# Performance work log

Measured on AMD Instinct MI355X. Metric: run time of the kernel, lower is better.

Reference implementation:

```python
import jax, jax.numpy as jnp
import numpy as np

N = 100000          # nodes
E = 1600000         # edges (avg degree 16)
F_IN = 35           # len(cfg.objects)
C = 21              # channels (out_channels)
DIMS = [F_IN, 16 * C, 8 * C, 4 * C, 2 * C]  # conv1..conv4 in-dims -> next
MAX_LOGSTD = 10.0


def setup_inputs() -> dict:
    key = jax.random.key(0)
    ks = jax.random.split(key, 16)
    inp = {
        "x": jax.random.normal(ks[0], (N, F_IN), dtype=jnp.float32),
        "edge_index": jax.random.randint(ks[1], (2, E), 0, N, dtype=jnp.int32),
        "eps": jax.random.normal(ks[2], (N, C), dtype=jnp.float32),
    }
    # GCNConv weights (glorot-ish scaling) and biases for conv1..conv4
    for i in range(4):
        din, dout = DIMS[i], DIMS[i + 1]
        inp[f"W{i+1}"] = jax.random.normal(ks[3 + i], (din, dout), dtype=jnp.float32) / np.sqrt(din)
        inp[f"b{i+1}"] = jnp.zeros((dout,), dtype=jnp.float32)
    # conv_mu / conv_logstd: 2*C -> C
    inp["W_mu"] = jax.random.normal(ks[8], (2 * C, C), dtype=jnp.float32) / np.sqrt(2 * C)
    inp["b_mu"] = jnp.zeros((C,), dtype=jnp.float32)
    inp["W_logstd"] = jax.random.normal(ks[9], (2 * C, C), dtype=jnp.float32) / np.sqrt(2 * C)
    inp["b_logstd"] = jnp.zeros((C,), dtype=jnp.float32)
    return inp


def _gcn_conv(x, src, dst, edge_norm, self_norm, W, b):
    # PyG GCNConv: linear transform first, then normalized scatter-add
    # (messages flow src -> dst, plus the self-loop term deg^-1/2 * deg^-1/2).
    h = x @ W                                            # [N, dout]
    msg = h[src] * edge_norm[:, None]                    # [E, dout] gather
    agg = jax.ops.segment_sum(msg, dst, num_segments=N)  # scatter-add
    agg = agg + h * self_norm[:, None]                   # self-loop contribution
    return agg + b


def reference(x, edge_index, eps, W1, b1, W2, b2, W3, b3, W4, b4,
              W_mu, b_mu, W_logstd, b_logstd):
    src, dst = edge_index[0], edge_index[1]
    # Symmetric normalization with self-loops: deg[i] = in_deg[i] + 1
    deg = jax.ops.segment_sum(jnp.ones((E,), x.dtype), dst, num_segments=N) + 1.0
    dinv = jax.lax.rsqrt(deg)                 # deg > 0 always (self loop)
    edge_norm = dinv[src] * dinv[dst]         # [E]
    self_norm = dinv * dinv                   # [N]

    h = jax.nn.relu(_gcn_conv(x, src, dst, edge_norm, self_norm, W1, b1))
    h = jax.nn.relu(_gcn_conv(h, src, dst, edge_norm, self_norm, W2, b2))
    h = jax.nn.relu(_gcn_conv(h, src, dst, edge_norm, self_norm, W3, b3))
    h = jax.nn.relu(_gcn_conv(h, src, dst, edge_norm, self_norm, W4, b4))

    mu = _gcn_conv(h, src, dst, edge_norm, self_norm, W_mu, b_mu)
    logstd = jnp.minimum(
        _gcn_conv(h, src, dst, edge_norm, self_norm, W_logstd, b_logstd),
        MAX_LOGSTD,
    )
    # VGAE reparameterize (training mode)
    z = mu + eps * jnp.exp(logstd)
    # Predictor
    p_z = jax.nn.log_softmax(z, axis=1)
    return p_z
```

## Files before the change

kernel.cpp:

```cpp
#include <hip/hip_runtime.h>

#define NN 100000
#define NE 1600000
#define MP 100096
#define NB 782
#define BSL 3072
#define CHUNK 8192

typedef short  short8 __attribute__((ext_vector_type(8)));
typedef float  f32x4  __attribute__((ext_vector_type(4)));
typedef float  f32x2  __attribute__((ext_vector_type(2)));

#if defined(__has_builtin)
# if __has_builtin(__builtin_amdgcn_cvt_pk_f32_fp8) && __has_builtin(__builtin_amdgcn_cvt_pk_fp8_f32)
#  define HW_FP8 1
# endif
#endif

__device__ __forceinline__ unsigned short f2bf(float f){
  unsigned int u = __float_as_uint(f);
  u += 0x7fffu + ((u >> 16) & 1u);
  return (unsigned short)(u >> 16);
}
__device__ __forceinline__ float bfl(unsigned int v){ return __uint_as_float((v & 0xffffu) << 16); }
__device__ __forceinline__ float bfh(unsigned int v){ return __uint_as_float(v & 0xffff0000u); }
__device__ __forceinline__ float bf1(unsigned short v){ return __uint_as_float(((unsigned int)v) << 16); }


__device__ __forceinline__ void dec4(unsigned int v, float f[4]){
#ifdef HW_FP8
  f32x2 lo = __builtin_amdgcn_cvt_pk_f32_fp8((int)v, false);
  f32x2 hi = __builtin_amdgcn_cvt_pk_f32_fp8((int)v, true);
  f[0] = lo[0]; f[1] = lo[1]; f[2] = hi[0]; f[3] = hi[1];
#else
  #pragma unroll
  for (int k = 0; k < 4; ++k){
    unsigned b = (v >> (8 * k)) & 0xffu;
    int em = b & 0x7f;
    float m = (em < 8) ? (float)em * 0.001953125f
                       : __uint_as_float((unsigned)((((em >> 3) + 120) << 23) | ((em & 7) << 20)));
    f[k] = (b & 0x80) ? -m : m;
  }
#endif
}

#ifndef HW_FP8
__device__ __forceinline__ unsigned int enc1m(float v){
  unsigned u = __float_as_uint(v);
  unsigned s = (u >> 24) & 0x80u;
  float av = fabsf(v);
  if (!(av >= 0.0009765625f)) return s;
  if (av >= 448.0f) return s | 0x7eu;
  if (av < 0.015625f){
    int q = (int)rintf(av * 512.0f);
    return s | (unsigned)q;
  }
  unsigned au = u & 0x7fffffffu;
  au += 0x7ffffu + ((au >> 20) & 1u);
  int ex = (int)(au >> 23) - 127;
  unsigned man = (au >> 20) & 7u;
  if (ex > 8) return s | 0x7eu;
  return s | (unsigned)((ex + 7) << 3) | man;
}
#endif

__device__ __forceinline__ unsigned int enc1(float v){
#ifdef HW_FP8
  return (unsigned int)__builtin_amdgcn_cvt_pk_fp8_f32(v, 0.0f, 0, false) & 0xffu;
#else
  return enc1m(v);
#endif
}

__device__ __forceinline__ unsigned int enc4(float a, float b, float c, float d){
#ifdef HW_FP8
  int lo = __builtin_amdgcn_cvt_pk_fp8_f32(a, b, 0, false);
  return (unsigned int)__builtin_amdgcn_cvt_pk_fp8_f32(c, d, lo, true);
#else
  return enc1m(a) | (enc1m(b) << 8) | (enc1m(c) << 16) | (enc1m(d) << 24);
#endif
}


__global__ __launch_bounds__(256) void k_bin1(const int* __restrict__ src, const int* __restrict__ dst,
                                              int* __restrict__ bcur, int2* __restrict__ tmp){
  __shared__ int cnt[NB];
  __shared__ int base[NB];
  __shared__ int pos[NB];
  int t = threadIdx.x;
  int e0 = blockIdx.x * CHUNK;
  int e1 = min(e0 + CHUNK, NE);
  for (int i = t; i < NB; i += 256){ cnt[i] = 0; pos[i] = 0; }
  __syncthreads();
  for (int e = e0 + t; e < e1; e += 256)
    atomicAdd(&cnt[dst[e] >> 7], 1);
  __syncthreads();
  for (int i = t; i < NB; i += 256){
    int c = cnt[i];
    base[i] = (c > 0) ? atomicAdd(&bcur[i], c) : 0;
  }
  __syncthreads();
  for (int e = e0 + t; e < e1; e += 256){
    int s = src[e], d = dst[e];
    int b = d >> 7;
    int p = b * BSL + base[b] + atomicAdd(&pos[b], 1);
    tmp[p] = make_int2(s, d);
  }
}

__global__ __launch_bounds__(256) void k_bscan(const int* __restrict__ bcur, int* __restrict__ bbase,
                                               int* __restrict__ rp){
  __shared__ int sh[256];
  int t = threadIdx.x;
  int b0 = t * 4;
  int v0 = (b0     < NB) ? bcur[b0]     : 0;
  int v1 = (b0 + 1 < NB) ? bcur[b0 + 1] : 0;
  int v2 = (b0 + 2 < NB) ? bcur[b0 + 2] : 0;
  int v3 = (b0 + 3 < NB) ? bcur[b0 + 3] : 0;
  int s = v0 + v1 + v2 + v3;
  sh[t] = s; __syncthreads();
  for (int off = 1; off < 256; off <<= 1){
    int val = sh[t];
    int add = (t >= off) ? sh[t - off] : 0;
    __syncthreads();
    sh[t] = val + add;
    __syncthreads();
  }
  int excl = sh[t] - s;
  if (b0     < NB) bbase[b0]     = excl;
  if (b0 + 1 < NB) bbase[b0 + 1] = excl + v0;
  if (b0 + 2 < NB) bbase[b0 + 2] = excl + v0 + v1;
  if (b0 + 3 < NB) bbase[b0 + 3] = excl + v0 + v1 + v2;
  if (t == 255){ bbase[NB] = sh[255]; rp[NN] = NE; }
}

__global__ __launch_bounds__(256) void k_bin2(const int2* __restrict__ tmp, const int* __restrict__ bbase,
                                              int* __restrict__ rp, float* __restrict__ dinv,
                                              int* __restrict__ cw){
  __shared__ int hist[128];
  __shared__ int cur[128];
  int b = blockIdx.x;
  int n0 = b << 7;
  int nn = min(128, NN - n0);
  int t = threadIdx.x;
  int B0 = bbase[b];
  int C  = bbase[b + 1] - B0;
  int E0 = b * BSL;
  if (t < 128) hist[t] = 0;
  __syncthreads();
  for (int e = t; e < C; e += 256)
    atomicAdd(&hist[tmp[E0 + e].y - n0], 1);
  __syncthreads();
  int val = (t < 128) ? hist[t] : 0;
  for (int off = 1; off < 128; off <<= 1){
    int add = (t < 128 && t >= off) ? hist[t - off] : 0;
    __syncthreads();
    if (t < 128) hist[t] += add;
    __syncthreads();
  }
  if (t < 128){
    int excl = hist[t] - val;
    int rpv = B0 + excl;
    cur[t] = rpv;
    if (t < nn){
      rp[n0 + t] = rpv;
      dinv[n0 + t] = rsqrtf((float)val + 1.0f);
    }
  }
  __syncthreads();
  for (int e = t; e < C; e += 256){
    int2 p = tmp[E0 + e];
    int slot = atomicAdd(&cur[p.y - n0], 1);
    cw[slot] = p.x;
  }
}


__device__ __forceinline__ void pack1(const float* __restrict__ W, unsigned short* __restrict__ dst,
                                      int din, int dout, int Np, int idx){
  int j = idx & 7;
  int l = (idx >> 3) & 63;
  int f = idx >> 9;
  int ntiles = Np >> 4;
  int nt = f % ntiles;
  int ks = f / ntiles;
  int k = ks * 32 + (l >> 4) * 8 + j;
  int n = nt * 16 + (l & 15);
  float v = (k < din && n < dout) ? W[k * dout + n] : 0.0f;
  dst[idx] = f2bf(v);
}

__global__ __launch_bounds__(256) void k_gxpack(const float* __restrict__ x, const float* __restrict__ dinv,
                                                unsigned int* __restrict__ gx,
                                                const float* __restrict__ W1, unsigned short* __restrict__ d1,
                                                const float* __restrict__ W2, unsigned short* __restrict__ d2,
                                                const float* __restrict__ W3, unsigned short* __restrict__ d3,
                                                const float* __restrict__ W4, unsigned short* __restrict__ d4){
  if (blockIdx.x < 6250){
    int idx = blockIdx.x * 256 + threadIdx.x;
    if (idx >= NN * 16) return;
    int row = idx >> 4;
    int cu  = idx & 15;
    float di = dinv[row];
    float v[4];
    #pragma unroll
    for (int k = 0; k < 4; ++k){
      int c = 4 * cu + k;
      v[k] = (c < 35) ? x[row * 35 + c] * di : 0.0f;
    }
    gx[idx] = enc4(v[0], v[1], v[2], v[3]);
  } else {
    int idx = (blockIdx.x - 6250) * 256 + threadIdx.x;
    if      (idx < 22528)  pack1(W1, d1, 35, 336, 352, idx);
    else if (idx < 90112)  pack1(W2, d2, 336, 168, 192, idx - 22528);
    else if (idx < 108544) pack1(W3, d3, 168, 84, 96, idx - 90112);
    else if (idx < 114688) pack1(W4, d4, 84, 42, 64, idx - 108544);
  }
}


template<int SPB, int OUTC, int DOUT, int MODE, int OUTF8>
__global__ __launch_bounds__(256) void k_aggf8(const unsigned char* __restrict__ Pin,
                                               void* __restrict__ Hout,
                                               const int* __restrict__ rp, const int* __restrict__ cw,
                                               const float* __restrict__ dinv, const float* __restrict__ bias){
  constexpr int L  = 16;
  constexpr int U  = SPB / 4;
  constexpr int CH = U / L;
  constexpr int UN = (CH == 1) ? 8 : 4;
  int g = blockIdx.x * 16 + (threadIdx.x >> 4);
  int c = threadIdx.x & 15;
  if (g >= NN) return;
  int e0 = rp[g], e1 = rp[g + 1];
  const unsigned int* __restrict__ P = (const unsigned int*)Pin;

  float a[CH][4];
  {
    const unsigned int* r = P + (size_t)g * U;
    #pragma unroll
    for (int ch = 0; ch < CH; ++ch) dec4(r[ch * L + c], a[ch]);
  }

  int e = e0;
  if (e + UN <= e1){
    int s[UN];
    #pragma unroll
    for (int u = 0; u < UN; ++u) s[u] = cw[e + u];
    while (true){
      unsigned int v[UN][CH];
      #pragma unroll
      for (int u = 0; u < UN; ++u){
        const unsigned int* r = P + (size_t)s[u] * U;
        #pragma unroll
        for (int ch = 0; ch < CH; ++ch) v[u][ch] = r[ch * L + c];
      }
      int e2 = e + UN;
      bool more = (e2 + UN <= e1);
      int s2[UN];
      if (more){
        #pragma unroll
        for (int u = 0; u < UN; ++u) s2[u] = cw[e2 + u];
      }
      #pragma unroll
      for (int u = 0; u < UN; ++u){
        #pragma unroll
        for (int ch = 0; ch < CH; ++ch){
          float f[4]; dec4(v[u][ch], f);
          a[ch][0] += f[0]; a[ch][1] += f[1]; a[ch][2] += f[2]; a[ch][3] += f[3];
        }
      }
      e = e2;
      if (!more) break;
      #pragma unroll
      for (int u = 0; u < UN; ++u) s[u] = s2[u];
    }
  }
  for (; e < e1; ++e){
    const unsigned int* r = P + (size_t)cw[e] * U;
    #pragma unroll
    for (int ch = 0; ch < CH; ++ch){
      float f[4]; dec4(r[ch * L + c], f);
      a[ch][0] += f[0]; a[ch][1] += f[1]; a[ch][2] += f[2]; a[ch][3] += f[3];
    }
  }

  float di = dinv[g];
  #pragma unroll
  for (int ch = 0; ch < CH; ++ch){
    int colbase = (ch * L + c) * 4;
    float f0 = a[ch][0] * di, f1 = a[ch][1] * di, f2 = a[ch][2] * di, f3 = a[ch][3] * di;
    if (MODE >= 1){
      f0 += (colbase     < DOUT) ? bias[colbase]     : 0.0f;
      f1 += (colbase + 1 < DOUT) ? bias[colbase + 1] : 0.0f;
      f2 += (colbase + 2 < DOUT) ? bias[colbase + 2] : 0.0f;
      f3 += (colbase + 3 < DOUT) ? bias[colbase + 3] : 0.0f;
      f0 = fmaxf(f0, 0.0f); f1 = fmaxf(f1, 0.0f);
      f2 = fmaxf(f2, 0.0f); f3 = fmaxf(f3, 0.0f);
      if (MODE == 2){ f0 *= di; f1 *= di; f2 *= di; f3 *= di; }
    }
    if (colbase < OUTC){
      if (OUTF8){
        unsigned int* orow = (unsigned int*)Hout + (size_t)g * (OUTC / 4);
        orow[ch * L + c] = enc4(f0, f1, f2, f3);
      } else {
        uint2* orow = (uint2*)Hout + (size_t)g * (OUTC / 4);
        uint2 o;
        o.x = (unsigned int)f2bf(f0) | ((unsigned int)f2bf(f1) << 16);
        o.y = (unsigned int)f2bf(f2) | ((unsigned int)f2bf(f3) << 16);
        orow[ch * L + c] = o;
      }
    }
  }
}


template<int K, int NP, int DOUT, int SPA, int EPI, int F8, int CSTB>
__global__ __launch_bounds__(256) void k_mm(const unsigned short* __restrict__ A,
                                            const unsigned short* __restrict__ Bp,
                                            const float* __restrict__ bias,
                                            const float* __restrict__ dinv,
                                            unsigned char* __restrict__ C){
  constexpr int NT  = NP / 16;
  constexpr int NT2 = NP / 32;
  int l   = threadIdx.x & 63;
  int wid = threadIdx.x >> 6;
  int wr = wid >> 1, wc = wid & 1;
  int r0 = blockIdx.x * 64 + wr * 32;
  int n0 = wc * (NP / 2);
  int lr = l & 15, lk = l >> 4;
  const short8* __restrict__ Af = (const short8*)A;
  const short8* __restrict__ Bf = (const short8*)Bp;
  f32x4 acc[2][NT2];
  #pragma unroll
  for (int m = 0; m < 2; ++m)
    #pragma unroll
    for (int t = 0; t < NT2; ++t) acc[m][t] = (f32x4){0.f, 0.f, 0.f, 0.f};

  for (int ks = 0; ks < K / 32; ++ks){
    short8 a0 = Af[((r0      + lr) * SPA + ks * 32 + lk * 8) >> 3];
    short8 a1 = Af[((r0 + 16 + lr) * SPA + ks * 32 + lk * 8) >> 3];
    const short8* bp = Bf + (ks * NT + (n0 >> 4)) * 64 + l;
    #pragma unroll
    for (int t = 0; t < NT2; ++t){
      short8 b = bp[t * 64];
      acc[0][t] = __builtin_amdgcn_mfma_f32_16x16x32_bf16(a0, b, acc[0][t], 0, 0, 0);
      acc[1][t] = __builtin_amdgcn_mfma_f32_16x16x32_bf16(a1, b, acc[1][t], 0, 0, 0);
    }
  }
  int rb = lk * 4;
  #pragma unroll
  for (int m = 0; m < 2; ++m){
    #pragma unroll
    for (int t = 0; t < NT2; ++t){
      int col = n0 + t * 16 + lr;
      float bv = 0.0f;
      if (EPI == 0) bv = (col < DOUT) ? bias[col] : 0.0f;
      #pragma unroll
      for (int j = 0; j < 4; ++j){
        int row = r0 + m * 16 + rb + j;
        if (row < NN){
          float v = acc[m][t][j];
          if (EPI == 0) v = fmaxf(v + bv, 0.0f);
          else          v = v * dinv[row];
          if (F8) C[(size_t)row * CSTB + col] = (unsigned char)enc1(v);
          else    *(unsigned short*)(C + (size_t)row * CSTB + 2 * col) = f2bf(v);
        }
      }
    }
  }
}


__global__ __launch_bounds__(256) void k_final(const unsigned short* __restrict__ aggh4,
                                               const float* __restrict__ Wmu, const float* __restrict__ bmu,
                                               const float* __restrict__ Wls, const float* __restrict__ bls,
                                               const float* __restrict__ eps, float* __restrict__ out){
  __shared__ float sWmu[42 * 21];
  __shared__ float sWls[42 * 21];
  __shared__ float sbmu[21];
  __shared__ float sbls[21];
  for (int u = threadIdx.x; u < 882; u += 256){ sWmu[u] = Wmu[u]; sWls[u] = Wls[u]; }
  if (threadIdx.x < 21){ sbmu[threadIdx.x] = bmu[threadIdx.x]; sbls[threadIdx.x] = bls[threadIdx.x]; }
  __syncthreads();

  int i = blockIdx.x * 256 + threadIdx.x;
  if (i >= NN) return;

  float mu[21], ls[21];
  #pragma unroll
  for (int j = 0; j < 21; ++j){ mu[j] = sbmu[j]; ls[j] = sbls[j]; }

  const unsigned short* arow = aggh4 + (size_t)i * 64;
  for (int k = 0; k < 42; ++k){
    float ak = bf1(arow[k]);
    #pragma unroll
    for (int j = 0; j < 21; ++j){
      mu[j] += ak * sWmu[k * 21 + j];
      ls[j] += ak * sWls[k * 21 + j];
    }
  }
  float zv[21];
  float mx = -3.4e38f;
  #pragma unroll
  for (int j = 0; j < 21; ++j){
    float l2 = fminf(ls[j], 10.0f);
    float zj = mu[j] + eps[(size_t)i * 21 + j] * __expf(l2);
    zv[j] = zj;
    mx = fmaxf(mx, zj);
  }
  float ssum = 0.f;
  #pragma unroll
  for (int j = 0; j < 21; ++j) ssum += __expf(zv[j] - mx);
  float lse = mx + __logf(ssum);
  #pragma unroll
  for (int j = 0; j < 21; ++j) out[(size_t)i * 21 + j] = zv[j] - lse;
}


constexpr size_t OFF_ROWPTR = 0;
constexpr size_t OFF_DINV   = 401408;
constexpr size_t OFF_BCUR   = 802816;
constexpr size_t OFF_BBASE  = 806400;
constexpr size_t OFF_CW     = 809984;
constexpr size_t OFF_TMP    = 7210496;
constexpr size_t OFF_WB1    = 26429440;
constexpr size_t OFF_WB2    = 26474496;
constexpr size_t OFF_WB3    = 26609664;
constexpr size_t OFF_WB4    = 26646528;
constexpr size_t OFF_GX     = 26659328;
constexpr size_t OFF_P2     = 26659328;
constexpr size_t OFF_Q4     = 26659328;
constexpr size_t OFF_AGGX   = 45878272;
constexpr size_t OFF_H1     = 58691072;
constexpr size_t OFF_H2     = 58691072;
constexpr size_t OFF_AGGH4  = 58691072;
constexpr size_t OFF_P3     = 129159168;
constexpr size_t OFF_P4     = 129159168;
constexpr size_t OFF_H3     = 141971968;

extern "C" void kernel_launch(void* const* d_in, const int* in_sizes, int n_in,
                              void* d_out, int out_size, void* d_ws, size_t ws_size,
                              hipStream_t stream){
  (void)in_sizes; (void)n_in; (void)out_size; (void)ws_size;
  const float* x    = (const float*)d_in[0];
  const int*   ei   = (const int*)d_in[1];
  const float* eps  = (const float*)d_in[2];
  const float* W1   = (const float*)d_in[3];  const float* b1  = (const float*)d_in[4];
  const float* W2   = (const float*)d_in[5];  const float* b2  = (const float*)d_in[6];
  const float* W3   = (const float*)d_in[7];  const float* b3  = (const float*)d_in[8];
  const float* W4   = (const float*)d_in[9];  const float* b4  = (const float*)d_in[10];
  const float* Wmu  = (const float*)d_in[11]; const float* bmu = (const float*)d_in[12];
  const float* Wls  = (const float*)d_in[13]; const float* bls = (const float*)d_in[14];

  char* ws = (char*)d_ws;
  int*   rowptr = (int*)(ws + OFF_ROWPTR);
  float* dinv   = (float*)(ws + OFF_DINV);
  int*   bcur   = (int*)(ws + OFF_BCUR);
  int*   bbase  = (int*)(ws + OFF_BBASE);
  int*   cw     = (int*)(ws + OFF_CW);
  int2*  tmp    = (int2*)(ws + OFF_TMP);
  unsigned short* wb1   = (unsigned short*)(ws + OFF_WB1);
  unsigned short* wb2   = (unsigned short*)(ws + OFF_WB2);
  unsigned short* wb3   = (unsigned short*)(ws + OFF_WB3);
  unsigned short* wb4   = (unsigned short*)(ws + OFF_WB4);
  unsigned char*  gx    = (unsigned char*)(ws + OFF_GX);
  unsigned short* aggx  = (unsigned short*)(ws + OFF_AGGX);
  unsigned short* h1    = (unsigned short*)(ws + OFF_H1);
  unsigned char*  p2    = (unsigned char*)(ws + OFF_P2);
  unsigned short* h2    = (unsigned short*)(ws + OFF_H2);
  unsigned char*  p3    = (unsigned char*)(ws + OFF_P3);
  unsigned short* h3    = (unsigned short*)(ws + OFF_H3);
  unsigned char*  p4    = (unsigned char*)(ws + OFF_P4);
  unsigned char*  q4    = (unsigned char*)(ws + OFF_Q4);
  unsigned short* aggh4 = (unsigned short*)(ws + OFF_AGGH4);

  const int* src = ei;
  const int* dst = ei + NE;

  hipMemsetAsync(bcur, 0, NB * sizeof(int), stream);
  k_bin1 <<<196, 256, 0, stream>>>(src, dst, bcur, tmp);
  k_bscan<<<1,   256, 0, stream>>>(bcur, bbase, rowptr);
  k_bin2 <<<NB,  256, 0, stream>>>(tmp, bbase, rowptr, dinv, cw);
  k_gxpack<<<6698, 256, 0, stream>>>(x, dinv, (unsigned int*)gx,
                                     W1, wb1, W2, wb2, W3, wb3, W4, wb4);

  k_aggf8<64, 64, 0, 0, 0><<<6250, 256, 0, stream>>>(gx, aggx, rowptr, cw, dinv, nullptr);
  k_mm<64, 352, 336, 64, 0, 0, 704><<<1564, 256, 0, stream>>>(aggx, wb1, b1, nullptr, (unsigned char*)h1);

  k_mm<352, 192, 168, 352, 1, 1, 192><<<1564, 256, 0, stream>>>(h1, wb2, nullptr, dinv, p2);
  k_aggf8<192, 192, 168, 1, 0><<<6250, 256, 0, stream>>>(p2, h2, rowptr, cw, dinv, b2);

  k_mm<192, 96, 84, 192, 1, 1, 128><<<1564, 256, 0, stream>>>(h2, wb3, nullptr, dinv, p3);
  k_aggf8<128, 96, 84, 1, 0><<<6250, 256, 0, stream>>>(p3, h3, rowptr, cw, dinv, b3);

  k_mm<96, 64, 42, 96, 1, 1, 64><<<1564, 256, 0, stream>>>(h3, wb4, nullptr, dinv, p4);
  k_aggf8<64, 64, 42, 2, 1><<<6250, 256, 0, stream>>>(p4, q4, rowptr, cw, dinv, b4);

  k_aggf8<64, 64, 0, 0, 0><<<6250, 256, 0, stream>>>(q4, aggh4, rowptr, cw, dinv, nullptr);

  k_final<<<391, 256, 0, stream>>>(aggh4, Wmu, bmu, Wls, bls, eps, (float*)d_out);
}
```

Baseline: 496.5 us.

## Fuse conv1 and conv2 matmuls through LDS and stage fp8 stores

Merges the conv1 dense transform (bias+ReLU) with the conv2 matmul into one kernel that keeps the 64x336 bf16 h1 tile in LDS, so the large h1 intermediate is never written to or read back from global memory. The remaining fp8 matmul epilogues now write to an LDS tile first and then copy out with coalesced 16-byte stores, replacing scattered single-byte global stores. This costs roughly 46KB of LDS per block for the fused kernel, which may limit occupancy, and adds extra barriers.

New measurement: 460.3 us. -7.3%, faster.

```diff
diff --git a/kernel.cpp b/kernel.cpp
--- a/kernel.cpp
+++ b/kernel.cpp
@@ -314,20 +314,123 @@
 }
 
 
-template<int K, int NP, int DOUT, int SPA, int EPI, int F8, int CSTB>
-__global__ __launch_bounds__(256) void k_mm(const unsigned short* __restrict__ A,
-                                            const unsigned short* __restrict__ Bp,
-                                            const float* __restrict__ bias,
-                                            const float* __restrict__ dinv,
-                                            unsigned char* __restrict__ C){
-  constexpr int NT  = NP / 16;
-  constexpr int NT2 = NP / 32;
+#define SROW 360
+
+__global__ __launch_bounds__(256) void k_conv12(const unsigned short* __restrict__ aggx,
+                                                const unsigned short* __restrict__ wb1,
+                                                const float* __restrict__ b1,
+                                                const unsigned short* __restrict__ wb2,
+                                                const float* __restrict__ dinv,
+                                                unsigned char* __restrict__ p2){
+  __shared__ uint4 ldsv[64 * SROW * 2 / 16];
+  unsigned short* h1t = (unsigned short*)ldsv;
+  unsigned char*  bts = (unsigned char*)ldsv;
+
   int l   = threadIdx.x & 63;
   int wid = threadIdx.x >> 6;
   int wr = wid >> 1, wc = wid & 1;
-  int r0 = blockIdx.x * 64 + wr * 32;
+  int lr = l & 15, lk = l >> 4;
+  int rb = lk * 4;
+  int R0 = blockIdx.x * 64;
+
+  {
+    int n0 = wc * 176;
+    const short8* __restrict__ Af = (const short8*)aggx;
+    const short8* __restrict__ Bf = (const short8*)wb1;
+    f32x4 acc[2][11];
+    #pragma unroll
+    for (int m = 0; m < 2; ++m)
+      #pragma unroll
+      for (int t = 0; t < 11; ++t) acc[m][t] = (f32x4){0.f, 0.f, 0.f, 0.f};
+    #pragma unroll
+    for (int ks = 0; ks < 2; ++ks){
+      short8 a0 = Af[((R0 + wr * 32      + lr) * 64 + ks * 32 + lk * 8) >> 3];
+      short8 a1 = Af[((R0 + wr * 32 + 16 + lr) * 64 + ks * 32 + lk * 8) >> 3];
+      const short8* bp = Bf + (ks * 22 + wc * 11) * 64 + l;
+      #pragma unroll
+      for (int t = 0; t < 11; ++t){
+        short8 b = bp[t * 64];
+        acc[0][t] = __builtin_amdgcn_mfma_f32_16x16x32_bf16(a0, b, acc[0][t], 0, 0, 0);
+        acc[1][t] = __builtin_amdgcn_mfma_f32_16x16x32_bf16(a1, b, acc[1][t], 0, 0, 0);
+      }
+    }
+    #pragma unroll
+    for (int m = 0; m < 2; ++m){
+      #pragma unroll
+      for (int t = 0; t < 11; ++t){
+        int col = n0 + t * 16 + lr;
+        float bv = (col < 336) ? b1[col] : 0.0f;
+        #pragma unroll
+        for (int j = 0; j < 4; ++j){
+          int rowl = wr * 32 + m * 16 + rb + j;
+          h1t[rowl * SROW + col] = f2bf(fmaxf(acc[m][t][j] + bv, 0.0f));
+        }
+      }
+    }
+  }
+  __syncthreads();
+
+  f32x4 acc2[2][6];
+  #pragma unroll
+  for (int m = 0; m < 2; ++m)
+    #pragma unroll
+    for (int t = 0; t < 6; ++t) acc2[m][t] = (f32x4){0.f, 0.f, 0.f, 0.f};
+  {
+    int n0 = wc * 96;
+    const short8* __restrict__ Bf = (const short8*)wb2;
+    for (int ks = 0; ks < 11; ++ks){
+      short8 a0 = *(const short8*)&h1t[(wr * 32      + lr) * SROW + ks * 32 + lk * 8];
+      short8 a1 = *(const short8*)&h1t[(wr * 32 + 16 + lr) * SROW + ks * 32 + lk * 8];
+      const short8* bp = Bf + (ks * 12 + wc * 6) * 64 + l;
+      #pragma unroll
+      for (int t = 0; t < 6; ++t){
+        short8 b = bp[t * 64];
+        acc2[0][t] = __builtin_amdgcn_mfma_f32_16x16x32_bf16(a0, b, acc2[0][t], 0, 0, 0);
+        acc2[1][t] = __builtin_amdgcn_mfma_f32_16x16x32_bf16(a1, b, acc2[1][t], 0, 0, 0);
+      }
+    }
+  }
+  __syncthreads();
+  {
+    int n0 = wc * 96;
+    #pragma unroll
+    for (int m = 0; m < 2; ++m){
+      #pragma unroll
+      for (int j = 0; j < 4; ++j){
+        int rowl = wr * 32 + m * 16 + rb + j;
+        float di = dinv[R0 + rowl];
+        #pragma unroll
+        for (int t = 0; t < 6; ++t)
+          bts[rowl * 208 + n0 + t * 16 + lr] = (unsigned char)enc1(acc2[m][t][j] * di);
+      }
+    }
+  }
+  __syncthreads();
+  for (int i = threadIdx.x; i < 768; i += 256){
+    int row = i / 12, off = (i % 12) * 16;
+    *(uint4*)&p2[(size_t)(R0 + row) * 192 + off] = *(const uint4*)&bts[row * 208 + off];
+  }
+}
+
+
+template<int K, int NP, int SPA, int CSTB>
+__global__ __launch_bounds__(256) void k_mmf8(const unsigned short* __restrict__ A,
+                                              const unsigned short* __restrict__ Bp,
+                                              const float* __restrict__ dinv,
+                                              unsigned char* __restrict__ C){
+  constexpr int NT   = NP / 16;
+  constexpr int NT2  = NP / 32;
+  constexpr int PSTR = CSTB + 16;
+  __shared__ uint4 ctv[64 * PSTR / 16];
+  unsigned char* ct = (unsigned char*)ctv;
+
+  int l   = threadIdx.x & 63;
+  int wid = threadIdx.x >> 6;
+  int wr = wid >> 1, wc = wid & 1;
+  int lr = l & 15, lk = l >> 4;
+  int rb = lk * 4;
+  int R0 = blockIdx.x * 64;
   int n0 = wc * (NP / 2);
-  int lr = l & 15, lk = l >> 4;
   const short8* __restrict__ Af = (const short8*)A;
   const short8* __restrict__ Bf = (const short8*)Bp;
   f32x4 acc[2][NT2];
@@ -337,8 +440,8 @@
     for (int t = 0; t < NT2; ++t) acc[m][t] = (f32x4){0.f, 0.f, 0.f, 0.f};
 
   for (int ks = 0; ks < K / 32; ++ks){
-    short8 a0 = Af[((r0      + lr) * SPA + ks * 32 + lk * 8) >> 3];
-    short8 a1 = Af[((r0 + 16 + lr) * SPA + ks * 32 + lk * 8) >> 3];
+    short8 a0 = Af[((R0 + wr * 32      + lr) * SPA + ks * 32 + lk * 8) >> 3];
+    short8 a1 = Af[((R0 + wr * 32 + 16 + lr) * SPA + ks * 32 + lk * 8) >> 3];
     const short8* bp = Bf + (ks * NT + (n0 >> 4)) * 64 + l;
     #pragma unroll
     for (int t = 0; t < NT2; ++t){
@@ -347,26 +450,29 @@
       acc[1][t] = __builtin_amdgcn_mfma_f32_16x16x32_bf16(a1, b, acc[1][t], 0, 0, 0);
     }
   }
-  int rb = lk * 4;
   #pragma unroll
   for (int m = 0; m < 2; ++m){
     #pragma unroll
-    for (int t = 0; t < NT2; ++t){
-      int col = n0 + t * 16 + lr;
-      float bv = 0.0f;
-      if (EPI == 0) bv = (col < DOUT) ? bias[col] : 0.0f;
-      #pragma unroll
-      for (int j = 0; j < 4; ++j){
-        int row = r0 + m * 16 + rb + j;
-        if (row < NN){
-          float v = acc[m][t][j];
-          if (EPI == 0) v = fmaxf(v + bv, 0.0f);
-          else          v = v * dinv[row];
-          if (F8) C[(size_t)row * CSTB + col] = (unsigned char)enc1(v);
-          else    *(unsigned short*)(C + (size_t)row * CSTB + 2 * col) = f2bf(v);
-        }
-      }
-    }
+    for (int j = 0; j < 4; ++j){
+      int rowl = wr * 32 + m * 16 + rb + j;
+      float di = dinv[R0 + rowl];
+      #pragma unroll
+      for (int t = 0; t < NT2; ++t)
+        ct[rowl * PSTR + n0 + t * 16 + lr] = (unsigned char)enc1(acc[m][t][j] * di);
+    }
+  }
+  if (CSTB > NP){
+    for (int i = threadIdx.x; i < 64 * (CSTB - NP) / 16; i += 256){
+      constexpr int PQ = (CSTB - NP) / 16;
+      int row = i / PQ, off = NP + (i % PQ) * 16;
+      *(uint4*)&ct[row * PSTR + off] = (uint4){0, 0, 0, 0};
+    }
+  }
+  __syncthreads();
+  constexpr int RQ = CSTB / 16;
+  for (int i = threadIdx.x; i < 64 * RQ; i += 256){
+    int row = i / RQ, off = (i % RQ) * 16;
+    *(uint4*)&C[(size_t)(R0 + row) * CSTB + off] = *(const uint4*)&ct[row * PSTR + off];
   }
 }
 
@@ -431,7 +537,6 @@
 constexpr size_t OFF_P2     = 26659328;
 constexpr size_t OFF_Q4     = 26659328;
 constexpr size_t OFF_AGGX   = 45878272;
-constexpr size_t OFF_H1     = 58691072;
 constexpr size_t OFF_H2     = 58691072;
 constexpr size_t OFF_AGGH4  = 58691072;
 constexpr size_t OFF_P3     = 129159168;
@@ -465,7 +570,6 @@
   unsigned short* wb4   = (unsigned short*)(ws + OFF_WB4);
   unsigned char*  gx    = (unsigned char*)(ws + OFF_GX);
   unsigned short* aggx  = (unsigned short*)(ws + OFF_AGGX);
-  unsigned short* h1    = (unsigned short*)(ws + OFF_H1);
   unsigned char*  p2    = (unsigned char*)(ws + OFF_P2);
   unsigned short* h2    = (unsigned short*)(ws + OFF_H2);
   unsigned char*  p3    = (unsigned char*)(ws + OFF_P3);
@@ -485,15 +589,14 @@
                                      W1, wb1, W2, wb2, W3, wb3, W4, wb4);
 
   k_aggf8<64, 64, 0, 0, 0><<<6250, 256, 0, stream>>>(gx, aggx, rowptr, cw, dinv, nullptr);
-  k_mm<64, 352, 336, 64, 0, 0, 704><<<1564, 256, 0, stream>>>(aggx, wb1, b1, nullptr, (unsigned char*)h1);
-
-  k_mm<352, 192, 168, 352, 1, 1, 192><<<1564, 256, 0, stream>>>(h1, wb2, nullptr, dinv, p2);
+  k_conv12<<<1564, 256, 0, stream>>>(aggx, wb1, b1, wb2, dinv, p2);
+
   k_aggf8<192, 192, 168, 1, 0><<<6250, 256, 0, stream>>>(p2, h2, rowptr, cw, dinv, b2);
 
-  k_mm<192, 96, 84, 192, 1, 1, 128><<<1564, 256, 0, stream>>>(h2, wb3, nullptr, dinv, p3);
+  k_mmf8<192, 96, 192, 128><<<1564, 256, 0, stream>>>(h2, wb3, dinv, p3);
   k_aggf8<128, 96, 84, 1, 0><<<6250, 256, 0, stream>>>(p3, h3, rowptr, cw, dinv, b3);
 
-  k_mm<96, 64, 42, 96, 1, 1, 64><<<1564, 256, 0, stream>>>(h3, wb4, nullptr, dinv, p4);
+  k_mmf8<96, 64, 96, 64><<<1564, 256, 0, stream>>>(h3, wb4, dinv, p4);
   k_aggf8<64, 64, 42, 2, 1><<<6250, 256, 0, stream>>>(p4, q4, rowptr, cw, dinv, b4);
 
   k_aggf8<64, 64, 0, 0, 0><<<6250, 256, 0, stream>>>(q4, aggh4, rowptr, cw, dinv, nullptr);
```
